# Kernel tuning notes

Hardware: AMD Instinct MI355X
Metric: run time of the kernel (lower is better)

The kernel has to match this reference:

```python
import jax, jax.numpy as jnp
import numpy as np

B, C, K, P = 32, 32, 3, 4
PSIZE = P * P
STRIDE = 2
EPS = 1e-8
BN_EPS = 1e-5


def _bn(x, scale, bias, mean, var):
    # eval-mode BatchNorm over channel-last axis
    return (x - mean) * (scale / jnp.sqrt(var + BN_EPS)) + bias


def setup_inputs() -> dict:
    key = jax.random.key(0)
    ks = jax.random.split(key, 13)
    b, h, w = 8, 64, 64
    c1_in, c1_out = C * K * K * 16, C * K * K      # 4608 -> 288
    c2_in, c2_out = C * K * K * 17, C * 17         # 4896 -> 544
    return {
        "x": jax.random.normal(ks[0], (b, B * (PSIZE + 1), h, w), jnp.float32),
        "weights": jax.random.normal(ks[1], (1, 1, C, B + 1), jnp.float32),
        "gamma": jax.random.normal(ks[2], (1, 1, 1, B, 1), jnp.float32),
        "conv1_w": jax.random.normal(ks[3], (c1_out, c1_in), jnp.float32) * 0.02,
        "bn1_scale": jax.random.uniform(ks[4], (c1_out,), jnp.float32) + 0.5,
        "bn1_bias": jax.random.normal(ks[5], (c1_out,), jnp.float32) * 0.1,
        "bn1_mean": jax.random.normal(ks[6], (c1_out,), jnp.float32) * 0.1,
        "bn1_var": jax.random.uniform(ks[7], (c1_out,), jnp.float32) + 0.5,
        "conv2_w": jax.random.normal(ks[8], (c2_out, c2_in), jnp.float32) * 0.02,
        "bn2_scale": jax.random.uniform(ks[9], (c2_out,), jnp.float32) + 0.5,
        "bn2_bias": jax.random.normal(ks[10], (c2_out,), jnp.float32) * 0.1,
        "bn2_mean": jax.random.normal(ks[11], (c2_out,), jnp.float32) * 0.1,
        "bn2_var": jax.random.uniform(ks[12], (c2_out,), jnp.float32) + 0.5,
    }


def reference(x, weights, gamma, conv1_w, bn1_scale, bn1_bias, bn1_mean, bn1_var,
              conv2_w, bn2_scale, bn2_bias, bn2_mean, bn2_var):
    b = x.shape[0]
    x = jnp.transpose(x, (0, 2, 3, 1))                       # (b,h,w,c)
    # add_pathes: zero-pad h,w by 1 then gather K*K overlapping patches
    x = jnp.pad(x, ((0, 0), (1, 1), (1, 1), (0, 0)))
    hp = x.shape[1]
    starts = np.arange(0, hp - K + 1, STRIDE)                # static
    idxs = starts[:, None] + np.arange(K)                    # (oh,K)
    oh = ow = int((hp - K) / STRIDE + 1)
    x = x[:, idxs]                                           # (b,oh,K,wp,c)
    x = x[:, :, :, idxs]                                     # (b,oh,K,ow,K,c)
    x = jnp.transpose(x, (0, 1, 3, 2, 4, 5))                 # (b,oh,ow,K,K,c)

    hw, kk = oh * ow, K * K
    p_in = x[..., :B * PSIZE].reshape(b, hw, kk, B, PSIZE)
    p_in = jnp.transpose(p_in, (0, 3, 1, 2, 4)).reshape(b, B, hw * kk * PSIZE)
    a_in = x[..., B * PSIZE:].reshape(b, hw, kk, B, 1)

    # transform_view: per-capsule-type normalization over all patches
    mu = p_in.mean(-1, keepdims=True)
    var = p_in.var(-1, ddof=1, keepdims=True)                # torch unbiased var
    p = (p_in - mu) / jnp.sqrt(var + EPS)                    # (b,B,N)
    p = jnp.transpose(p, (0, 2, 1)).reshape(b, hw, kk, B, PSIZE)
    p = a_in * p * gamma                                     # activation+gamma gating
    gsm = jax.nn.softmax(gamma, axis=3)                      # softmax over B
    psum = jnp.sum(p * gsm, axis=3, keepdims=True)           # (b,hw,kk,1,PSIZE)
    p = jnp.concatenate([p, psum], axis=3)                   # (b,hw,kk,B+1,PSIZE)
    w_sm = jax.nn.softmax(weights, axis=2)[0, 0]             # (C,B+1), softmax over C
    p_out = jnp.einsum('cd,bhkdp->bhkcp', w_sm, p)           # (b,hw,kk,C,PSIZE)
    p_out = p_out.reshape(b, oh, ow, kk * C * PSIZE)         # channels-last, 4608

    # conv1: 1x1 conv + BN + sigmoid
    a = jnp.einsum('bhwc,oc->bhwo', p_out, conv1_w)
    a = jax.nn.sigmoid(_bn(a, bn1_scale, bn1_bias, bn1_mean, bn1_var))
    out = jnp.concatenate([p_out, a], axis=3)                # 4896 channels
    # conv2: 1x1 conv + BN + relu
    y = jnp.einsum('bhwc,oc->bhwo', out, conv2_w)
    y = jax.nn.relu(_bn(y, bn2_scale, bn2_bias, bn2_mean, bn2_var))
    return jnp.transpose(y, (0, 3, 1, 2))                    # (b, C*17, oh, ow)
```

## Files before the change

kernel.cpp:

```cpp
#include <hip/hip_runtime.h>
#include <math.h>


typedef unsigned short u16;
typedef __attribute__((ext_vector_type(8))) short short8;
typedef __attribute__((ext_vector_type(4))) float f32x4;
typedef __attribute__((ext_vector_type(16))) float f32x16;

#define MFMA16(a, b, c) __builtin_amdgcn_mfma_f32_16x16x32_bf16(a, b, c, 0, 0, 0)
#define MFMA32(a, b, c) __builtin_amdgcn_mfma_f32_32x32x16_bf16(a, b, c, 0, 0, 0)
#define SB0() __builtin_amdgcn_sched_barrier(0)

#define LN_EPS 1e-8f

#define O_MU    0
#define O_RSTD  256
#define O_W2    512
#define O_BN1S  1536
#define O_BN1B  1824
#define O_BN2S  2112
#define O_BN2B  2656
#define O_ZB    3200

#define O_G_B     16384ull
#define O_AACT_B  (O_G_B + 33554432ull)
#define O_PART_B  (O_AACT_B + 5242880ull)
#define O_WF_B    (O_PART_B + 17825792ull)
#define O_WA_B    (O_WF_B + 9437184ull)

__device__ __forceinline__ u16 f2bf(float f) {
  union { float f; unsigned u; } v; v.f = f;
  unsigned r = (v.u + 0x7fffu + ((v.u >> 16) & 1u)) >> 16;
  return (u16)r;
}

__device__ __forceinline__ void gll16(const void* g, void* l) {
  __builtin_amdgcn_global_load_lds(
      (const __attribute__((address_space(1))) unsigned int*)g,
      (__attribute__((address_space(3))) unsigned int*)l, 16, 0, 0);
}

__device__ __forceinline__ int sfun(int r) { return (r >> 1) & 3; }

__global__ __launch_bounds__(256) void prep_kernel(
    const float* __restrict__ wts, const float* __restrict__ gamma,
    const float* __restrict__ bn1s, const float* __restrict__ bn1bi,
    const float* __restrict__ bn1m, const float* __restrict__ bn1v,
    const float* __restrict__ bn2s, const float* __restrict__ bn2bi,
    const float* __restrict__ bn2m, const float* __restrict__ bn2v,
    float* __restrict__ ws)
{
  __shared__ float wsm[32 * 33];
  __shared__ float gs[32];
  int t = threadIdx.x;
  if (t < 33) {
    float mx = -1e30f;
    for (int c = 0; c < 32; ++c) mx = fmaxf(mx, wts[c * 33 + t]);
    float sum = 0.f;
    for (int c = 0; c < 32; ++c) {
      float e = expf(wts[c * 33 + t] - mx);
      wsm[c * 33 + t] = e; sum += e;
    }
    float inv = 1.f / sum;
    for (int c = 0; c < 32; ++c) wsm[c * 33 + t] *= inv;
  }
  if (t == 64) {
    float mx = -1e30f;
    for (int d = 0; d < 32; ++d) mx = fmaxf(mx, gamma[d]);
    for (int d = 0; d < 32; ++d) { float e = expf(gamma[d] - mx); gs[d] = e; }
    float sum = 0.f;
    for (int d = 0; d < 32; ++d) sum += gs[d];
    float inv = 1.f / sum;
    for (int d = 0; d < 32; ++d) gs[d] *= inv;
  }
  __syncthreads();
  for (int i = t; i < 1024; i += 256) {
    int c = i >> 5, d = i & 31;
    ws[O_W2 + i] = (wsm[c * 33 + d] + wsm[c * 33 + 32] * gs[d]) * gamma[d];
  }
  for (int i = t; i < 288; i += 256) {
    float s = bn1s[i] / sqrtf(bn1v[i] + 1e-5f);
    ws[O_BN1S + i] = s;
    ws[O_BN1B + i] = bn1bi[i] - bn1m[i] * s;
  }
  for (int i = t; i < 544; i += 256) {
    float s = bn2s[i] / sqrtf(bn2v[i] + 1e-5f);
    ws[O_BN2S + i] = s;
    ws[O_BN2B + i] = bn2bi[i] - bn2m[i] * s;
  }
  if (t < 64) ws[O_ZB + t] = 0.f;
}

__global__ __launch_bounds__(1024) void stats_kernel(
    const float* __restrict__ x, float* __restrict__ ws, u16* __restrict__ Aact)
{
  int g = blockIdx.x;
  int b = g >> 5, cb = g & 31;
  const float* base = x + (((size_t)(b * 544 + cb * 16)) << 12);
  float s = 0.f, q = 0.f;
  for (int idx = threadIdx.x; idx < 65536; idx += 1024) {
    int p = idx & 4095;
    int hi = p >> 6, wi = p & 63;
    float wh = ((hi & 1) && hi != 63) ? 2.f : 1.f;
    float ww = ((wi & 1) && wi != 63) ? 2.f : 1.f;
    float v = base[idx];
    float wgt = wh * ww;
    s += wgt * v;
    q += wgt * v * v;
  }
  __shared__ float sb[1024], qb[1024];
  int t = threadIdx.x;
  sb[t] = s; qb[t] = q;
  __syncthreads();
  for (int off = 512; off > 0; off >>= 1) {
    if (t < off) { sb[t] += sb[t + off]; qb[t] += qb[t + off]; }
    __syncthreads();
  }
  if (t == 0) {
    const float N = 147456.f;
    float mean = sb[0] / N;
    float var = (qb[0] - sb[0] * sb[0] / N) / (N - 1.f);
    ws[O_MU + g] = mean;
    ws[O_RSTD + g] = 1.f / sqrtf(var + LN_EPS);
  }
  {
    int pos = (g << 5) + (t >> 5);
    Aact[(size_t)pos * 320 + 288 + (t & 31)] = 0;
  }
}

__global__ __launch_bounds__(256) void wcvt_kernel(
    const float* __restrict__ w1, const float* __restrict__ w2,
    u16* __restrict__ Wf, u16* __restrict__ Wa)
{
  int sid = blockIdx.x * 256 + threadIdx.x;
  if (sid < 589824) {
    int nt = sid / 73728, rem = sid - nt * 73728;
    int ch = rem / 512, r2 = rem - ch * 512;
    int c = r2 >> 2, p = r2 & 3;
    int o = nt * 128 + c;
    int q = p ^ ((c >> 1) & 3);
    int kf = (ch << 5) + (q << 3);
    u16* dst = Wf + (size_t)sid * 8;
#pragma unroll
    for (int e = 0; e < 8; ++e) {
      int k = kf + e;
      float v = 0.f;
      if (o < 288) v = w1[(size_t)o * 4608 + k];
      else if (o < 832) v = w2[(size_t)(o - 288) * 4896 + k];
      dst[e] = f2bf(v);
    }
  } else if (sid < 612864) {
    int s2 = sid - 589824;
    int cb = s2 / 768, si = s2 - cb * 768;
    int ob = cb / 5, ch = cb - ob * 5;
    int nt = si >> 8, ks = (si >> 6) & 3, l2 = si & 63;
    int o = ob * 96 + (nt << 5) + (l2 & 31);
    int kf = (ch << 6) + (ks << 4) + ((l2 >> 5) << 3);
    u16* dst = Wa + (size_t)s2 * 8;
#pragma unroll
    for (int e = 0; e < 8; ++e) {
      int k = kf + e;
      float v = (o < 544 && k < 288) ? w2[(size_t)o * 4896 + 4608 + k] : 0.f;
      dst[e] = f2bf(v);
    }
  }
}

__global__ __launch_bounds__(256) void g_kernel(
    const float* __restrict__ x, const float* __restrict__ ws,
    u16* __restrict__ Gb)
{
  __shared__ __align__(16) float raw[16][545];
  __shared__ __align__(16) float ut[16][576];
  __shared__ float w2s[1024];
  __shared__ float mus[32], rss[32];
  int t = threadIdx.x;
  int pb = blockIdx.x;
  int b = pb >> 8, hi = (pb >> 2) & 63, wi0 = (pb & 3) << 4;

  {
    int ch4 = t >> 2, wl4 = (t & 3) << 2;
    size_t gbase = ((size_t)b * 544) << 12;
    size_t rowoff = ((size_t)hi << 6) + (size_t)(wi0 + wl4);
    for (int it = 0; it < 9; ++it) {
      int ch = it * 64 + ch4;
      if (ch < 544) {
        float4 v = *reinterpret_cast<const float4*>(
            &x[gbase + ((size_t)ch << 12) + rowoff]);
        raw[wl4 + 0][ch] = v.x;
        raw[wl4 + 1][ch] = v.y;
        raw[wl4 + 2][ch] = v.z;
        raw[wl4 + 3][ch] = v.w;
      }
    }
  }
  for (int i = t; i < 1024; i += 256) w2s[i] = ws[O_W2 + i];
  if (t < 32) { mus[t] = ws[O_MU + b * 32 + t]; rss[t] = ws[O_RSTD + b * 32 + t]; }
  __syncthreads();

  {
    int dl = t & 15, psp = t >> 4;
    for (int it = 0; it < 32; ++it) {
      int pix = it >> 1, half = it & 1;
      int dp = half * 16 + dl;
      int j = (dp << 4) + psp;
      int cbv = j & 31, psv = j >> 5;
      float val = (raw[pix][(cbv << 4) + psv] - mus[cbv]) * rss[cbv];
      ut[pix][psp * 36 + dp] = raw[pix][512 + dp] * val;
    }
  }
  __syncthreads();

  {
    int c0 = t >> 4, psp = t & 15;
    float w2a[32], w2b[32];
#pragma unroll
    for (int d = 0; d < 32; ++d) {
      w2a[d] = w2s[c0 * 32 + d];
      w2b[d] = w2s[(c0 + 16) * 32 + d];
    }
    u16* Gp = Gb + ((size_t)((((b << 6) + hi) << 6) + wi0)) * 512;
    for (int pix = 0; pix < 16; ++pix) {
      float acc0 = 0.f, acc1 = 0.f;
      const float* up = &ut[pix][psp * 36];
#pragma unroll
      for (int k = 0; k < 8; ++k) {
        float4 u4 = *reinterpret_cast<const float4*>(up + 4 * k);
        acc0 = fmaf(w2a[4 * k + 0], u4.x, acc0);
        acc0 = fmaf(w2a[4 * k + 1], u4.y, acc0);
        acc0 = fmaf(w2a[4 * k + 2], u4.z, acc0);
        acc0 = fmaf(w2a[4 * k + 3], u4.w, acc0);
        acc1 = fmaf(w2b[4 * k + 0], u4.x, acc1);
        acc1 = fmaf(w2b[4 * k + 1], u4.y, acc1);
        acc1 = fmaf(w2b[4 * k + 2], u4.z, acc1);
        acc1 = fmaf(w2b[4 * k + 3], u4.w, acc1);
      }
      u16* gp = Gp + (size_t)pix * 512;
      gp[t] = f2bf(acc0);
      gp[256 + t] = f2bf(acc1);
    }
  }
}

__global__ __launch_bounds__(256) void gemm_fused(
    const u16* __restrict__ Gb, const u16* __restrict__ Wf,
    const float* __restrict__ wsf, u16* __restrict__ Aact,
    float* __restrict__ partC2)
{
  __shared__ __align__(16) u16 AlA[3][4096];
  __shared__ __align__(16) u16 AlB[3][4096];
  const int t = threadIdx.x;
  const int w = t >> 6, l = t & 63;
  const int wtm = w & 1, wtn = w >> 1;
  int bx = blockIdx.x;
  int xcd = bx & 7, idx = bx >> 3;
  int mloc = idx & 7, nt = idx >> 3;
  int mt = (xcd << 3) + mloc;
  int p0 = mt << 7;

  size_t pixb[2]; int hb[2], wb[2], qa[2], dof[2];
#pragma unroll
  for (int g = 0; g < 2; ++g) {
    int r = (w << 5) + (g << 4) + (l >> 2);
    int pos = p0 + r;
    int b_ = pos >> 10, h_ = (pos >> 5) & 31, w_ = pos & 31;
    pixb[g] = ((size_t)b_) << 12;
    hb[g] = 2 * h_ - 1;
    wb[g] = 2 * w_ - 1;
    qa[g] = (((l & 3) ^ sfun(r)) << 3);
    dof[g] = ((w << 5) + (g << 4)) * 32 + (l << 3);
  }
  const u16* zb = (const u16*)(wsf + O_ZB);
  const u16* wfslab = Wf + ((size_t)(nt * 144)) * 4096;

  int aoffs[4], boffs[4];
#pragma unroll
  for (int f = 0; f < 4; ++f) {
    int r = (wtm << 6) + (f << 4) + (l & 15);
    aoffs[f] = r * 32 + ((((l >> 4)) ^ sfun(r)) << 3);
    int c = (wtn << 6) + (f << 4) + (l & 15);
    boffs[f] = c * 32 + ((((l >> 4)) ^ sfun(c)) << 3);
  }

  f32x4 acc[4][4];
#pragma unroll
  for (int i = 0; i < 4; ++i)
#pragma unroll
    for (int j = 0; j < 4; ++j) acc[i][j] = (f32x4){0.f, 0.f, 0.f, 0.f};

  auto stage = [&](int ch, int buf) {
    int tap = ch >> 4;
    int kh = tap / 3, kw = tap - kh * 3;
    int cbase = (ch & 15) << 5;
#pragma unroll
    for (int g = 0; g < 2; ++g) {
      int hi = hb[g] + kh, wi = wb[g] + kw;
      bool ok = ((unsigned)hi < 64u) && ((unsigned)wi < 64u);
      const u16* src = ok
          ? (Gb + ((pixb[g] + ((size_t)hi << 6) + (size_t)wi) << 9) + cbase + qa[g])
          : (zb + qa[g]);
      gll16(src, &AlA[buf][dof[g]]);
    }
    const u16* wsrc = wfslab + ((size_t)ch << 12);
#pragma unroll
    for (int g = 0; g < 2; ++g)
      gll16(wsrc + dof[g], &AlB[buf][dof[g]]);
  };

  stage(0, 0);
  stage(1, 1);

  int buf = 0;
  for (int n = 0; n < 144; ++n) {
    SB0();
    if (n < 143) asm volatile("s_waitcnt vmcnt(4)" ::: "memory");
    else         asm volatile("s_waitcnt vmcnt(0)" ::: "memory");
    SB0();
    __builtin_amdgcn_s_barrier();
    SB0();
    if (n + 2 < 144) {
      int nb = (buf >= 1) ? buf - 1 : 2;
      stage(n + 2, nb);
    }
    SB0();
    short8 aF[4], bF[4];
#pragma unroll
    for (int f = 0; f < 4; ++f) {
      aF[f] = *(const short8*)&AlA[buf][aoffs[f]];
      bF[f] = *(const short8*)&AlB[buf][boffs[f]];
    }
    __builtin_amdgcn_s_setprio(1);
#pragma unroll
    for (int fm = 0; fm < 4; ++fm)
#pragma unroll
      for (int fn = 0; fn < 4; ++fn)
        acc[fm][fn] = MFMA16(aF[fm], bF[fn], acc[fm][fn]);
    __builtin_amdgcn_s_setprio(0);
    buf = (buf == 2) ? 0 : buf + 1;
  }

  const float* s1 = wsf + O_BN1S;
  const float* b1 = wsf + O_BN1B;
#pragma unroll
  for (int fn = 0; fn < 4; ++fn) {
    int o = nt * 128 + (wtn << 6) + (fn << 4) + (l & 15);
    if (o < 288) {
      float sc = s1[o], bi = b1[o];
#pragma unroll
      for (int fm = 0; fm < 4; ++fm) {
        int posr = p0 + (wtm << 6) + (fm << 4) + ((l >> 4) << 2);
#pragma unroll
        for (int r = 0; r < 4; ++r) {
          float z = acc[fm][fn][r] * sc + bi;
          float sg = 1.f / (1.f + expf(-z));
          Aact[(size_t)(posr + r) * 320 + o] = f2bf(sg);
        }
      }
    } else if (o < 832) {
#pragma unroll
      for (int fm = 0; fm < 4; ++fm) {
        int posr = p0 + (wtm << 6) + (fm << 4) + ((l >> 4) << 2);
#pragma unroll
        for (int r = 0; r < 4; ++r)
          partC2[(size_t)(posr + r) * 544 + (o - 288)] = acc[fm][fn][r];
      }
    }
  }
}

__global__ __launch_bounds__(256, 2) void gemm_act(
    const u16* __restrict__ Aact, const u16* __restrict__ Wa,
    const float* __restrict__ partial, const float* __restrict__ wsf,
    float* __restrict__ outp)
{
  __shared__ __align__(16) char lraw[57344];
  u16 (*AlA)[128 * 64] = (u16 (*)[128 * 64])lraw;
  u16 (*AlB)[6144] = (u16 (*)[6144])(lraw + 32768);
  float* T = (float*)lraw;
  const int t = threadIdx.x;
  const int wid = t >> 6, l = t & 63;
  int bx = blockIdx.x;
  int xcd = bx & 7, idx = bx >> 3;
  int mt = xcd + ((idx & 7) << 3);
  int ob = idx >> 3;
  int p0 = mt << 7;

  const u16* abase[4];
  int srow[4];
#pragma unroll
  for (int s = 0; s < 4; ++s) {
    int r = (wid << 5) + (s << 3) + (l >> 3);
    int jsw = ((l & 7) ^ (r & 7)) << 3;
    srow[s] = (wid << 5) + (s << 3);
    abase[s] = Aact + (size_t)(p0 + r) * 320 + jsw;
  }
  const u16* wslice = Wa + (size_t)(ob * 5) * 6144;
  const int bsub = (wid << 9) + (l << 3);

  f32x16 acc0 = {}, acc1 = {}, acc2 = {};

  auto stageA = [&](int ch, u16* lbuf) {
#pragma unroll
    for (int s = 0; s < 4; ++s)
      gll16(abase[s] + (ch << 6), lbuf + (srow[s] << 6));
  };
  auto stageB = [&](int ch, u16* lbuf) {
    const u16* src = wslice + (size_t)ch * 6144 + bsub;
#pragma unroll
    for (int c = 0; c < 3; ++c)
      gll16(src + (c << 11), lbuf + (c << 11) + (wid << 9));
  };
  const int rr = (wid << 5) + (l & 31);
  auto ldsA = [&](const u16* lbuf, short8* av) {
#pragma unroll
    for (int ks = 0; ks < 4; ++ks) {
      int jl = (ks << 1) + (l >> 5);
      av[ks] = *(const short8*)(lbuf + (rr << 6) + ((jl ^ (rr & 7)) << 3));
    }
  };
  auto ldsB = [&](const u16* lbuf, short8* bf) {
#pragma unroll
    for (int k2 = 0; k2 < 12; ++k2)
      bf[k2] = *(const short8*)(lbuf + (k2 << 9) + (l << 3));
  };
  auto mfmaR = [&](const short8* av, const short8* bf) {
    __builtin_amdgcn_s_setprio(1);
#pragma unroll
    for (int ks = 0; ks < 4; ++ks) {
      acc0 = MFMA32(av[ks], bf[ks], acc0);
      acc1 = MFMA32(av[ks], bf[4 + ks], acc1);
      acc2 = MFMA32(av[ks], bf[8 + ks], acc2);
    }
    __builtin_amdgcn_s_setprio(0);
  };

  short8 av[4], bf[12];

  stageA(0, AlA[0]);
  stageB(0, AlB[0]);
  asm volatile("s_waitcnt vmcnt(0)" ::: "memory");
  __builtin_amdgcn_s_barrier();

#define APHASE(K, CUR, NXT)                                                   \
  SB0();                                                                      \
  if ((K) + 1 < 5) { stageA((K) + 1, AlA[NXT]); stageB((K) + 1, AlB[NXT]); }  \
  SB0();                                                                      \
  ldsA(AlA[CUR], av);                                                         \
  ldsB(AlB[CUR], bf);                                                         \
  SB0();                                                                      \
  mfmaR(av, bf);                                                              \
  SB0();                                                                      \
  asm volatile("s_waitcnt vmcnt(0)" ::: "memory");                            \
  __builtin_amdgcn_s_barrier();

  APHASE(0, 0, 1);
  APHASE(1, 1, 0);
  APHASE(2, 0, 1);
  APHASE(3, 1, 0);
  APHASE(4, 0, 1);
#undef APHASE

  __syncthreads();

  const float* s2p = wsf + O_BN2S;
  const float* b2p = wsf + O_BN2B;
#pragma unroll
  for (int nt = 0; nt < 3; ++nt) {
    int ol = (nt << 5) + (l & 31);
    int o = ob * 96 + ol;
    float sc = 0.f, bi = 0.f;
    if (o < 544) { sc = s2p[o]; bi = b2p[o]; }
    f32x16 a = (nt == 0) ? acc0 : ((nt == 1) ? acc1 : acc2);
#pragma unroll
    for (int reg = 0; reg < 16; ++reg) {
      int rowD = (reg & 3) + ((reg >> 2) << 3) + ((l >> 5) << 2);
      int pos = p0 + (wid << 5) + rowD;
      float pz = 0.f;
      if (o < 544) pz = partial[(size_t)pos * 544 + o];
      float z = (a[reg] + pz) * sc + bi;
      T[ol * 129 + (wid << 5) + rowD] = fmaxf(z, 0.f);
    }
  }
  __syncthreads();
  for (int s2 = t; s2 < 3072; s2 += 256) {
    int ol = s2 >> 5, c4 = s2 & 31;
    int o = ob * 96 + ol;
    if (o < 544) {
      int pos0 = p0 + (c4 << 2);
      int bb = pos0 >> 10, hw0 = pos0 & 1023;
      int base = ol * 129 + (c4 << 2);
      float4 v;
      v.x = T[base]; v.y = T[base + 1]; v.z = T[base + 2]; v.w = T[base + 3];
      *(float4*)&outp[(((size_t)(bb * 544 + o)) << 10) + hw0] = v;
    }
  }
}

extern "C" void kernel_launch(void* const* d_in, const int* in_sizes, int n_in,
                              void* d_out, int out_size, void* d_ws,
                              size_t ws_size, hipStream_t stream)
{
  const float* x       = (const float*)d_in[0];
  const float* wts     = (const float*)d_in[1];
  const float* gamma   = (const float*)d_in[2];
  const float* conv1_w = (const float*)d_in[3];
  const float* bn1s    = (const float*)d_in[4];
  const float* bn1b    = (const float*)d_in[5];
  const float* bn1m    = (const float*)d_in[6];
  const float* bn1v    = (const float*)d_in[7];
  const float* conv2_w = (const float*)d_in[8];
  const float* bn2s    = (const float*)d_in[9];
  const float* bn2b    = (const float*)d_in[10];
  const float* bn2m    = (const float*)d_in[11];
  const float* bn2v    = (const float*)d_in[12];

  char* wsb = (char*)d_ws;
  float* wsf = (float*)d_ws;
  u16* Gb    = (u16*)(wsb + O_G_B);
  u16* Aact  = (u16*)(wsb + O_AACT_B);
  float* prt = (float*)(wsb + O_PART_B);
  u16* Wf    = (u16*)(wsb + O_WF_B);
  u16* Wa    = (u16*)(wsb + O_WA_B);
  float* out = (float*)d_out;

  prep_kernel<<<1, 256, 0, stream>>>(wts, gamma, bn1s, bn1b, bn1m, bn1v,
                                     bn2s, bn2b, bn2m, bn2v, wsf);
  stats_kernel<<<256, 1024, 0, stream>>>(x, wsf, Aact);
  wcvt_kernel<<<2394, 256, 0, stream>>>(conv1_w, conv2_w, Wf, Wa);
  g_kernel<<<2048, 256, 0, stream>>>(x, wsf, Gb);
  gemm_fused<<<512, 256, 0, stream>>>(Gb, Wf, wsf, Aact, prt);
  gemm_act<<<384, 256, 0, stream>>>(Aact, Wa, prt, wsf, out);
}
```

Baseline: 215.2 us.

## Fold capsule-mixing weight matrix into conv weights instead of per-pixel compute

The 32x33 softmax mixing matrix (w_sm/gamma) is no longer applied per pixel in g_kernel. It is folded into the conv1/conv2 weight slab inside wcvt_kernel, which now computes W·w2 per output row and tap. g_kernel now only normalizes, gates and packs the raw activations to bf16. This removes the per-pixel 32x32 FMA work, at the cost of a larger weight-prep kernel (9216 blocks) and a separate launch for the Wa conversion. Rounding changes because the product is formed in fp32 and then rounded once.

```diff
diff --git a/kernel.cpp b/kernel.cpp
--- a/kernel.cpp
+++ b/kernel.cpp
@@ -131,49 +131,76 @@
 
 __global__ __launch_bounds__(256) void wcvt_kernel(
     const float* __restrict__ w1, const float* __restrict__ w2,
-    u16* __restrict__ Wf, u16* __restrict__ Wa)
-{
-  int sid = blockIdx.x * 256 + threadIdx.x;
-  if (sid < 589824) {
-    int nt = sid / 73728, rem = sid - nt * 73728;
-    int ch = rem / 512, r2 = rem - ch * 512;
-    int c = r2 >> 2, p = r2 & 3;
-    int o = nt * 128 + c;
-    int q = p ^ ((c >> 1) & 3);
-    int kf = (ch << 5) + (q << 3);
-    u16* dst = Wf + (size_t)sid * 8;
-#pragma unroll
-    for (int e = 0; e < 8; ++e) {
-      int k = kf + e;
-      float v = 0.f;
-      if (o < 288) v = w1[(size_t)o * 4608 + k];
-      else if (o < 832) v = w2[(size_t)(o - 288) * 4896 + k];
-      dst[e] = f2bf(v);
-    }
-  } else if (sid < 612864) {
-    int s2 = sid - 589824;
-    int cb = s2 / 768, si = s2 - cb * 768;
-    int ob = cb / 5, ch = cb - ob * 5;
-    int nt = si >> 8, ks = (si >> 6) & 3, l2 = si & 63;
-    int o = ob * 96 + (nt << 5) + (l2 & 31);
-    int kf = (ch << 6) + (ks << 4) + ((l2 >> 5) << 3);
-    u16* dst = Wa + (size_t)s2 * 8;
-#pragma unroll
-    for (int e = 0; e < 8; ++e) {
-      int k = kf + e;
-      float v = (o < 544 && k < 288) ? w2[(size_t)o * 4896 + 4608 + k] : 0.f;
-      dst[e] = f2bf(v);
-    }
+    const float* __restrict__ wsf, u16* __restrict__ Wf)
+{
+  __shared__ float rowl[512];
+  __shared__ float w2l[1024];
+  int bid = blockIdx.x;
+  int o = bid / 9, tap = bid - (bid / 9) * 9;
+  int t = threadIdx.x;
+  int nt = o >> 7, cc = o & 127;
+  if (o < 832) {
+    const float* src = (o < 288)
+        ? (w1 + (size_t)o * 4608 + tap * 512)
+        : (w2 + (size_t)(o - 288) * 4896 + tap * 512);
+    rowl[t] = src[t];
+    rowl[t + 256] = src[t + 256];
+    w2l[t] = wsf[O_W2 + t];
+    w2l[t + 256] = wsf[O_W2 + t + 256];
+    w2l[t + 512] = wsf[O_W2 + t + 512];
+    w2l[t + 768] = wsf[O_W2 + t + 768];
+    __syncthreads();
+#pragma unroll
+    for (int i = 0; i < 2; ++i) {
+      int j = (t << 1) + i;
+      int d = j >> 4, ps = j & 15;
+      float s = 0.f;
+#pragma unroll
+      for (int c = 0; c < 32; ++c)
+        s = fmaf(rowl[(c << 4) + ps], w2l[(c << 5) + d], s);
+      int ch = (tap << 4) + (j >> 5);
+      int kin = j & 31;
+      int p = (kin >> 3) ^ ((cc >> 1) & 3);
+      size_t idx = ((((size_t)(nt * 144 + ch)) * 128 + cc) * 4 + p) * 8 + (kin & 7);
+      Wf[idx] = f2bf(s);
+    }
+  } else {
+#pragma unroll
+    for (int i = 0; i < 2; ++i) {
+      int j = (t << 1) + i;
+      int ch = (tap << 4) + (j >> 5);
+      int kin = j & 31;
+      int p = (kin >> 3) ^ ((cc >> 1) & 3);
+      size_t idx = ((((size_t)(nt * 144 + ch)) * 128 + cc) * 4 + p) * 8 + (kin & 7);
+      Wf[idx] = 0;
+    }
+  }
+}
+
+__global__ __launch_bounds__(256) void wa_cvt_kernel(
+    const float* __restrict__ w2, u16* __restrict__ Wa)
+{
+  int s2 = blockIdx.x * 256 + threadIdx.x;
+  int cb = s2 / 768, si = s2 - cb * 768;
+  int ob = cb / 5, ch = cb - ob * 5;
+  int nt = si >> 8, ks = (si >> 6) & 3, l2 = si & 63;
+  int o = ob * 96 + (nt << 5) + (l2 & 31);
+  int kf = (ch << 6) + (ks << 4) + ((l2 >> 5) << 3);
+  u16* dst = Wa + (size_t)s2 * 8;
+#pragma unroll
+  for (int e = 0; e < 8; ++e) {
+    int k = kf + e;
+    float v = (o < 544 && k < 288) ? w2[(size_t)o * 4896 + 4608 + k] : 0.f;
+    dst[e] = f2bf(v);
   }
 }
 
 __global__ __launch_bounds__(256) void g_kernel(
     const float* __restrict__ x, const float* __restrict__ ws,
-    u16* __restrict__ Gb)
+    u16* __restrict__ Ub)
 {
   __shared__ __align__(16) float raw[16][545];
   __shared__ __align__(16) float ut[16][576];
-  __shared__ float w2s[1024];
   __shared__ float mus[32], rss[32];
   int t = threadIdx.x;
   int pb = blockIdx.x;
@@ -195,7 +222,6 @@
       }
     }
   }
-  for (int i = t; i < 1024; i += 256) w2s[i] = ws[O_W2 + i];
   if (t < 32) { mus[t] = ws[O_MU + b * 32 + t]; rss[t] = ws[O_RSTD + b * 32 + t]; }
   __syncthreads();
 
@@ -213,38 +239,21 @@
   __syncthreads();
 
   {
-    int c0 = t >> 4, psp = t & 15;
-    float w2a[32], w2b[32];
-#pragma unroll
-    for (int d = 0; d < 32; ++d) {
-      w2a[d] = w2s[c0 * 32 + d];
-      w2b[d] = w2s[(c0 + 16) * 32 + d];
-    }
-    u16* Gp = Gb + ((size_t)((((b << 6) + hi) << 6) + wi0)) * 512;
+    u16* Up = Ub + ((size_t)((((b << 6) + hi) << 6) + wi0)) * 512;
+    int j0 = t << 1;
+    int a0 = (j0 & 15) * 36 + (j0 >> 4);
+    int a1 = ((j0 + 1) & 15) * 36 + ((j0 + 1) >> 4);
     for (int pix = 0; pix < 16; ++pix) {
-      float acc0 = 0.f, acc1 = 0.f;
-      const float* up = &ut[pix][psp * 36];
-#pragma unroll
-      for (int k = 0; k < 8; ++k) {
-        float4 u4 = *reinterpret_cast<const float4*>(up + 4 * k);
-        acc0 = fmaf(w2a[4 * k + 0], u4.x, acc0);
-        acc0 = fmaf(w2a[4 * k + 1], u4.y, acc0);
-        acc0 = fmaf(w2a[4 * k + 2], u4.z, acc0);
-        acc0 = fmaf(w2a[4 * k + 3], u4.w, acc0);
-        acc1 = fmaf(w2b[4 * k + 0], u4.x, acc1);
-        acc1 = fmaf(w2b[4 * k + 1], u4.y, acc1);
-        acc1 = fmaf(w2b[4 * k + 2], u4.z, acc1);
-        acc1 = fmaf(w2b[4 * k + 3], u4.w, acc1);
-      }
-      u16* gp = Gp + (size_t)pix * 512;
-      gp[t] = f2bf(acc0);
-      gp[256 + t] = f2bf(acc1);
+      float v0 = ut[pix][a0];
+      float v1 = ut[pix][a1];
+      unsigned pack = (unsigned)f2bf(v0) | ((unsigned)f2bf(v1) << 16);
+      *reinterpret_cast<unsigned*>(Up + (size_t)pix * 512 + j0) = pack;
     }
   }
 }
 
 __global__ __launch_bounds__(256) void gemm_fused(
-    const u16* __restrict__ Gb, const u16* __restrict__ Wf,
+    const u16* __restrict__ Ubp, const u16* __restrict__ Wf,
     const float* __restrict__ wsf, u16* __restrict__ Aact,
     float* __restrict__ partC2)
 {
@@ -298,7 +307,7 @@
       int hi = hb[g] + kh, wi = wb[g] + kw;
       bool ok = ((unsigned)hi < 64u) && ((unsigned)wi < 64u);
       const u16* src = ok
-          ? (Gb + ((pixb[g] + ((size_t)hi << 6) + (size_t)wi) << 9) + cbase + qa[g])
+          ? (Ubp + ((pixb[g] + ((size_t)hi << 6) + (size_t)wi) << 9) + cbase + qa[g])
           : (zb + qa[g]);
       gll16(src, &AlA[buf][dof[g]]);
     }
@@ -517,7 +526,7 @@
 
   char* wsb = (char*)d_ws;
   float* wsf = (float*)d_ws;
-  u16* Gb    = (u16*)(wsb + O_G_B);
+  u16* Ub    = (u16*)(wsb + O_G_B);
   u16* Aact  = (u16*)(wsb + O_AACT_B);
   float* prt = (float*)(wsb + O_PART_B);
   u16* Wf    = (u16*)(wsb + O_WF_B);
@@ -527,8 +536,9 @@
   prep_kernel<<<1, 256, 0, stream>>>(wts, gamma, bn1s, bn1b, bn1m, bn1v,
                                      bn2s, bn2b, bn2m, bn2v, wsf);
   stats_kernel<<<256, 1024, 0, stream>>>(x, wsf, Aact);
-  wcvt_kernel<<<2394, 256, 0, stream>>>(conv1_w, conv2_w, Wf, Wa);
-  g_kernel<<<2048, 256, 0, stream>>>(x, wsf, Gb);
-  gemm_fused<<<512, 256, 0, stream>>>(Gb, Wf, wsf, Aact, prt);
+  wcvt_kernel<<<9216, 256, 0, stream>>>(conv1_w, conv2_w, wsf, Wf);
+  wa_cvt_kernel<<<90, 256, 0, stream>>>(conv2_w, Wa);
+  g_kernel<<<2048, 256, 0, stream>>>(x, wsf, Ub);
+  gemm_fused<<<512, 256, 0, stream>>>(Ub, Wf, wsf, Aact, prt);
   gemm_act<<<384, 256, 0, stream>>>(Aact, Wa, prt, wsf, out);
 }
```

Measured after the change: 205.5 us, median of 2. 1.05x faster.
